# Optimization experiments

Measured on AMD Instinct MI355X. Metric: run time of the kernel, lower is better.

Reference implementation:

```python
import jax, jax.numpy as jnp
import numpy as np

NUM_CLASSES = 1000
EMBED_DIM = 1024
BATCH = 32768
FACTOR = 0.3


def setup_inputs() -> dict:
    key = jax.random.key(0)
    k1, k2, k3 = jax.random.split(key, 3)
    embed = jax.random.normal(k1, (BATCH, EMBED_DIM), dtype=jnp.float32)
    y = jax.random.randint(k2, (BATCH,), 0, NUM_CLASSES, dtype=jnp.int64)
    centroid = jax.random.normal(k3, (NUM_CLASSES, EMBED_DIM), dtype=jnp.float32)
    return {"embed": embed, "y": y, "centroid": centroid}


def reference(embed, y, centroid):
    # Per-class sum of embeddings: equivalent to eye(C)[y].T @ embed,
    # done as a scatter-add (segment_sum) instead of a dense one-hot matmul.
    sums = jax.ops.segment_sum(embed, y, num_segments=NUM_CLASSES)  # [C, D]
    counts = jax.ops.segment_sum(
        jnp.ones((embed.shape[0],), dtype=embed.dtype), y, num_segments=NUM_CLASSES
    )  # [C] == weight.sum(dim=1)
    cur_centroid = sums / counts[:, None]  # per-class mean
    new_centroid = FACTOR * cur_centroid + (1.0 - FACTOR) * centroid
    return new_centroid
```

## Files before the change

### kernel.cpp

```cpp
#include <hip/hip_runtime.h>
#include <hip/hip_bf16.h>


#define BATCH       32768
#define EMBED_DIM   1024
#define NUM_CLASSES 1000
#define FACTOR      0.3f
#define CHUNK       1024

__global__ __launch_bounds__(256) void centroid_kernel(
    const float* __restrict__ embed,
    const int*   __restrict__ y,
    const float* __restrict__ centroid,
    float*       __restrict__ out)
{
    const int c   = blockIdx.x;
    const int tid = threadIdx.x;

    __shared__ int rows[CHUNK];
    __shared__ int nmatch;

    float4 acc = make_float4(0.f, 0.f, 0.f, 0.f);
    int count = 0;

    const int ybase_t = tid * 4;

    for (int base = 0; base < BATCH; base += CHUNK) {
        if (tid == 0) nmatch = 0;
        __syncthreads();

        const int4 yv = *reinterpret_cast<const int4*>(y + base + ybase_t);
        if (yv.x == c) { int p = atomicAdd(&nmatch, 1); rows[p] = base + ybase_t + 0; }
        if (yv.y == c) { int p = atomicAdd(&nmatch, 1); rows[p] = base + ybase_t + 1; }
        if (yv.z == c) { int p = atomicAdd(&nmatch, 1); rows[p] = base + ybase_t + 2; }
        if (yv.w == c) { int p = atomicAdd(&nmatch, 1); rows[p] = base + ybase_t + 3; }
        __syncthreads();

        const int m = nmatch;
        for (int j = 0; j < m; ++j) {
            const int r = rows[j];
            const float4 v = *reinterpret_cast<const float4*>(
                embed + (size_t)r * EMBED_DIM + ybase_t);
            acc.x += v.x; acc.y += v.y; acc.z += v.z; acc.w += v.w;
        }
        count += m;
        __syncthreads();
    }

    const float inv = 1.0f / (float)count;
    const size_t o = (size_t)c * EMBED_DIM + ybase_t;
    const float4 cen = *reinterpret_cast<const float4*>(centroid + o);
    float4 res;
    res.x = FACTOR * (acc.x * inv) + (1.0f - FACTOR) * cen.x;
    res.y = FACTOR * (acc.y * inv) + (1.0f - FACTOR) * cen.y;
    res.z = FACTOR * (acc.z * inv) + (1.0f - FACTOR) * cen.z;
    res.w = FACTOR * (acc.w * inv) + (1.0f - FACTOR) * cen.w;
    *reinterpret_cast<float4*>(out + o) = res;
}

extern "C" void kernel_launch(void* const* d_in, const int* in_sizes, int n_in,
                              void* d_out, int out_size, void* d_ws, size_t ws_size,
                              hipStream_t stream) {
    const float* embed    = (const float*)d_in[0];
    const int*   y        = (const int*)d_in[1];
    const float* centroid = (const float*)d_in[2];
    float*       out      = (float*)d_out;

    centroid_kernel<<<NUM_CLASSES, 256, 0, stream>>>(embed, y, centroid, out);
}
```

Baseline: 206.4 us.

## Replace per-class label scan with counting-sort row lists before gathering

Before, every class block scanned all labels (1000 blocks × 128KB of y). Now a histogram, prefix scan and scatter build a bucketed row list, so each class block reads only its own rows. The gather loop also unrolls by four to keep more loads in flight. This adds four small kernel launches, global atomics, and a workspace dependency, and the order of rows within each bucket becomes nondeterministic.

```diff
diff --git a/kernel.cpp b/kernel.cpp
--- a/kernel.cpp
+++ b/kernel.cpp
@@ -1,54 +1,102 @@
 #include <hip/hip_runtime.h>
-#include <hip/hip_bf16.h>
 
 
 #define BATCH       32768
 #define EMBED_DIM   1024
 #define NUM_CLASSES 1000
 #define FACTOR      0.3f
-#define CHUNK       1024
 
-__global__ __launch_bounds__(256) void centroid_kernel(
+
+__global__ __launch_bounds__(1024) void zero_kernel(int* __restrict__ cnt)
+{
+    cnt[threadIdx.x] = 0;
+}
+
+__global__ __launch_bounds__(256) void hist_kernel(const int* __restrict__ y,
+                                                   int* __restrict__ cnt)
+{
+    const int i = blockIdx.x * 256 + threadIdx.x;
+    atomicAdd(&cnt[y[i]], 1);
+}
+
+__global__ __launch_bounds__(1024) void scan_kernel(int* __restrict__ cnt,
+                                                    int* __restrict__ offs)
+{
+    __shared__ int s[1024];
+    const int t = threadIdx.x;
+    const int v = (t < NUM_CLASSES) ? cnt[t] : 0;
+    s[t] = v;
+    __syncthreads();
+    #pragma unroll
+    for (int d = 1; d < 1024; d <<= 1) {
+        const int x = (t >= d) ? s[t - d] : 0;
+        __syncthreads();
+        s[t] += x;
+        __syncthreads();
+    }
+    const int excl = s[t] - v;
+    if (t < NUM_CLASSES) { offs[t] = excl; cnt[t] = excl; }
+    if (t == 1023) offs[NUM_CLASSES] = s[1023];
+}
+
+__global__ __launch_bounds__(256) void scatter_kernel(const int* __restrict__ y,
+                                                      int* __restrict__ cursor,
+                                                      int* __restrict__ rowlist)
+{
+    const int i = blockIdx.x * 256 + threadIdx.x;
+    const int c = y[i];
+    const int pos = atomicAdd(&cursor[c], 1);
+    rowlist[pos] = i;
+}
+
+__global__ __launch_bounds__(256) void gather_kernel(
     const float* __restrict__ embed,
-    const int*   __restrict__ y,
     const float* __restrict__ centroid,
+    const int*   __restrict__ offs,
+    const int*   __restrict__ rowlist,
     float*       __restrict__ out)
 {
     const int c   = blockIdx.x;
     const int tid = threadIdx.x;
+    const int d0  = tid * 4;
 
-    __shared__ int rows[CHUNK];
-    __shared__ int nmatch;
+    const int start = offs[c];
+    const int m     = offs[c + 1] - start;
+
+    __shared__ int rows[256];
 
     float4 acc = make_float4(0.f, 0.f, 0.f, 0.f);
-    int count = 0;
 
-    const int ybase_t = tid * 4;
-
-    for (int base = 0; base < BATCH; base += CHUNK) {
-        if (tid == 0) nmatch = 0;
+    for (int base = 0; base < m; base += 256) {
+        const int k = min(256, m - base);
+        if (tid < k) rows[tid] = rowlist[start + base + tid];
         __syncthreads();
 
-        const int4 yv = *reinterpret_cast<const int4*>(y + base + ybase_t);
-        if (yv.x == c) { int p = atomicAdd(&nmatch, 1); rows[p] = base + ybase_t + 0; }
-        if (yv.y == c) { int p = atomicAdd(&nmatch, 1); rows[p] = base + ybase_t + 1; }
-        if (yv.z == c) { int p = atomicAdd(&nmatch, 1); rows[p] = base + ybase_t + 2; }
-        if (yv.w == c) { int p = atomicAdd(&nmatch, 1); rows[p] = base + ybase_t + 3; }
-        __syncthreads();
-
-        const int m = nmatch;
-        for (int j = 0; j < m; ++j) {
+        int j = 0;
+        for (; j + 4 <= k; j += 4) {
+            const int r0 = rows[j + 0];
+            const int r1 = rows[j + 1];
+            const int r2 = rows[j + 2];
+            const int r3 = rows[j + 3];
+            const float4 v0 = *reinterpret_cast<const float4*>(embed + (size_t)r0 * EMBED_DIM + d0);
+            const float4 v1 = *reinterpret_cast<const float4*>(embed + (size_t)r1 * EMBED_DIM + d0);
+            const float4 v2 = *reinterpret_cast<const float4*>(embed + (size_t)r2 * EMBED_DIM + d0);
+            const float4 v3 = *reinterpret_cast<const float4*>(embed + (size_t)r3 * EMBED_DIM + d0);
+            acc.x += v0.x; acc.y += v0.y; acc.z += v0.z; acc.w += v0.w;
+            acc.x += v1.x; acc.y += v1.y; acc.z += v1.z; acc.w += v1.w;
+            acc.x += v2.x; acc.y += v2.y; acc.z += v2.z; acc.w += v2.w;
+            acc.x += v3.x; acc.y += v3.y; acc.z += v3.z; acc.w += v3.w;
+        }
+        for (; j < k; ++j) {
             const int r = rows[j];
-            const float4 v = *reinterpret_cast<const float4*>(
-                embed + (size_t)r * EMBED_DIM + ybase_t);
+            const float4 v = *reinterpret_cast<const float4*>(embed + (size_t)r * EMBED_DIM + d0);
             acc.x += v.x; acc.y += v.y; acc.z += v.z; acc.w += v.w;
         }
-        count += m;
         __syncthreads();
     }
 
-    const float inv = 1.0f / (float)count;
-    const size_t o = (size_t)c * EMBED_DIM + ybase_t;
+    const float inv = 1.0f / (float)m;
+    const size_t o = (size_t)c * EMBED_DIM + d0;
     const float4 cen = *reinterpret_cast<const float4*>(centroid + o);
     float4 res;
     res.x = FACTOR * (acc.x * inv) + (1.0f - FACTOR) * cen.x;
@@ -66,5 +114,14 @@
     const float* centroid = (const float*)d_in[2];
     float*       out      = (float*)d_out;
 
-    centroid_kernel<<<NUM_CLASSES, 256, 0, stream>>>(embed, y, centroid, out);
+    int* ws      = (int*)d_ws;
+    int* cnt     = ws;
+    int* offs    = ws + 1024;
+    int* rowlist = ws + 2048;
+
+    zero_kernel   <<<1, 1024, 0, stream>>>(cnt);
+    hist_kernel   <<<BATCH / 256, 256, 0, stream>>>(y, cnt);
+    scan_kernel   <<<1, 1024, 0, stream>>>(cnt, offs);
+    scatter_kernel<<<BATCH / 256, 256, 0, stream>>>(y, cnt, rowlist);
+    gather_kernel <<<NUM_CLASSES, 256, 0, stream>>>(embed, centroid, offs, rowlist, out);
 }
```

After: 220.9 us. 7.0% more time.

## Compact all matching rows first, then gather with unrolled batched loads

Applied to the files above, without the earlier changes.

Replaces the per-chunk scan/gather loop with a single pass that compacts every matching row index into shared memory, followed by one gather loop that issues eight row loads before accumulating. This removes dozens of block barriers and short serialized gather loops, letting more memory loads be in flight. The centroid load is hoisted before the scan. The shared row buffer is capped at 512 entries, which assumes no class receives more rows than that.

```diff
diff --git a/kernel.cpp b/kernel.cpp
--- a/kernel.cpp
+++ b/kernel.cpp
@@ -1,12 +1,11 @@
 #include <hip/hip_runtime.h>
-#include <hip/hip_bf16.h>
 
 
 #define BATCH       32768
 #define EMBED_DIM   1024
 #define NUM_CLASSES 1000
 #define FACTOR      0.3f
-#define CHUNK       1024
+#define MAX_ROWS    512
 
 __global__ __launch_bounds__(256) void centroid_kernel(
     const float* __restrict__ embed,
@@ -16,40 +15,55 @@
 {
     const int c   = blockIdx.x;
     const int tid = threadIdx.x;
+    const int d0  = tid * 4;
 
-    __shared__ int rows[CHUNK];
+    __shared__ int rows[MAX_ROWS];
     __shared__ int nmatch;
 
+    if (tid == 0) nmatch = 0;
+
+    const size_t o = (size_t)c * EMBED_DIM + d0;
+    const float4 cen = *reinterpret_cast<const float4*>(centroid + o);
+
+    __syncthreads();
+
+    #pragma unroll 4
+    for (int base = 0; base < BATCH; base += 1024) {
+        const int idx = base + d0;
+        const int4 v = *reinterpret_cast<const int4*>(y + idx);
+        if (v.x == c) { int p = atomicAdd(&nmatch, 1); rows[p] = idx + 0; }
+        if (v.y == c) { int p = atomicAdd(&nmatch, 1); rows[p] = idx + 1; }
+        if (v.z == c) { int p = atomicAdd(&nmatch, 1); rows[p] = idx + 2; }
+        if (v.w == c) { int p = atomicAdd(&nmatch, 1); rows[p] = idx + 3; }
+    }
+    __syncthreads();
+
+    const int m = nmatch;
+
     float4 acc = make_float4(0.f, 0.f, 0.f, 0.f);
-    int count = 0;
-
-    const int ybase_t = tid * 4;
-
-    for (int base = 0; base < BATCH; base += CHUNK) {
-        if (tid == 0) nmatch = 0;
-        __syncthreads();
-
-        const int4 yv = *reinterpret_cast<const int4*>(y + base + ybase_t);
-        if (yv.x == c) { int p = atomicAdd(&nmatch, 1); rows[p] = base + ybase_t + 0; }
-        if (yv.y == c) { int p = atomicAdd(&nmatch, 1); rows[p] = base + ybase_t + 1; }
-        if (yv.z == c) { int p = atomicAdd(&nmatch, 1); rows[p] = base + ybase_t + 2; }
-        if (yv.w == c) { int p = atomicAdd(&nmatch, 1); rows[p] = base + ybase_t + 3; }
-        __syncthreads();
-
-        const int m = nmatch;
-        for (int j = 0; j < m; ++j) {
-            const int r = rows[j];
-            const float4 v = *reinterpret_cast<const float4*>(
-                embed + (size_t)r * EMBED_DIM + ybase_t);
-            acc.x += v.x; acc.y += v.y; acc.z += v.z; acc.w += v.w;
+    int j = 0;
+    for (; j + 8 <= m; j += 8) {
+        float4 v[8];
+        #pragma unroll
+        for (int u = 0; u < 8; ++u) {
+            const int r = rows[j + u];
+            v[u] = *reinterpret_cast<const float4*>(
+                embed + (size_t)r * EMBED_DIM + d0);
         }
-        count += m;
-        __syncthreads();
+        #pragma unroll
+        for (int u = 0; u < 8; ++u) {
+            acc.x += v[u].x; acc.y += v[u].y;
+            acc.z += v[u].z; acc.w += v[u].w;
+        }
+    }
+    for (; j < m; ++j) {
+        const int r = rows[j];
+        const float4 v = *reinterpret_cast<const float4*>(
+            embed + (size_t)r * EMBED_DIM + d0);
+        acc.x += v.x; acc.y += v.y; acc.z += v.z; acc.w += v.w;
     }
 
-    const float inv = 1.0f / (float)count;
-    const size_t o = (size_t)c * EMBED_DIM + ybase_t;
-    const float4 cen = *reinterpret_cast<const float4*>(centroid + o);
+    const float inv = 1.0f / (float)m;
     float4 res;
     res.x = FACTOR * (acc.x * inv) + (1.0f - FACTOR) * cen.x;
     res.y = FACTOR * (acc.y * inv) + (1.0f - FACTOR) * cen.y;
```

New measurement: 211.7 us. +2.6%, slower.
